# Kernel optimization log

Measured on AMD Instinct MI355X. Metric: run time of the kernel, lower is better.

The kernel has to match this reference:

```python
import jax, jax.numpy as jnp
import numpy as np

B, S, E = 4, 2048, 1024
H, D = 16, 64
SCALE = D ** -0.5


def setup_inputs() -> dict:
    key = jax.random.key(0)
    ks = jax.random.split(key, 9)
    std = E ** -0.5
    return {
        "hidden_states": jax.random.normal(ks[0], (B, S, E), jnp.float32),
        "Wq": jax.random.normal(ks[1], (E, E), jnp.float32) * std,
        "bq": jax.random.normal(ks[2], (E,), jnp.float32) * 0.02,
        "Wk": jax.random.normal(ks[3], (E, E), jnp.float32) * std,
        "bk": jax.random.normal(ks[4], (E,), jnp.float32) * 0.02,
        "Wv": jax.random.normal(ks[5], (E, E), jnp.float32) * std,
        "bv": jax.random.normal(ks[6], (E,), jnp.float32) * 0.02,
        "Wo": jax.random.normal(ks[7], (E, E), jnp.float32) * std,
        "bo": jax.random.normal(ks[8], (E,), jnp.float32) * 0.02,
    }


def reference(hidden_states, Wq, bq, Wk, bk, Wv, bv, Wo, bo):
    b, s, e = hidden_states.shape
    # projections (torch Linear: x @ W^T + b); query pre-scaled as in source
    q = (hidden_states @ Wq.T + bq) * SCALE
    k = hidden_states @ Wk.T + bk
    v = hidden_states @ Wv.T + bv
    # [b, s, h, d] -> [b, h, s, d]
    q = q.reshape(b, s, H, D).transpose(0, 2, 1, 3)
    k = k.reshape(b, s, H, D).transpose(0, 2, 1, 3)
    v = v.reshape(b, s, H, D).transpose(0, 2, 1, 3)
    # explicit QK^T, fp32 softmax (matches source: softmax in float32 then cast back)
    scores = jnp.einsum("bhqd,bhkd->bhqk", q, k)
    attn = jax.nn.softmax(scores.astype(jnp.float32), axis=-1).astype(q.dtype)
    out = jnp.einsum("bhqk,bhkd->bhqd", attn, v)
    out = out.transpose(0, 2, 1, 3).reshape(b, s, e)
    return out @ Wo.T + bo
```

## Files before the change

kernel.cpp:

```cpp
#include <hip/hip_runtime.h>
#include <hip/hip_bf16.h>

#define BB 4
#define SS 2048
#define EE 1024
#define HH 16
#define DD 64
static constexpr float SCALE = 0.125f;

typedef __attribute__((ext_vector_type(8))) short bf16x8;
typedef __attribute__((ext_vector_type(4))) float f32x4;

#define MFMA(a, b, c) __builtin_amdgcn_mfma_f32_16x16x32_bf16(a, b, c, 0, 0, 0)

#define GLDS16(gptr, lptr) __builtin_amdgcn_global_load_lds( \
    (const __attribute__((address_space(1))) unsigned int*)(gptr), \
    (__attribute__((address_space(3))) unsigned int*)(lptr), 16, 0, 0)

__device__ inline unsigned short f2bfu(float f) {
    __hip_bfloat16 h = __float2bfloat16(f);
    return *reinterpret_cast<unsigned short*>(&h);
}

#define NX4 2097152
#define NW4 262144
#define NT4 (NX4 + 4 * NW4)
__global__ __launch_bounds__(256) void cast_all(
    const float* __restrict__ X,  const float* __restrict__ Wq,
    const float* __restrict__ Wk, const float* __restrict__ Wv,
    const float* __restrict__ Wo, unsigned short* __restrict__ dst) {
    for (int i = blockIdx.x * 256 + threadIdx.x; i < NT4; i += gridDim.x * 256) {
        const float* src; int off;
        if (i < NX4)               { src = X;  off = i; }
        else if (i < NX4 + NW4)    { src = Wq; off = i - NX4; }
        else if (i < NX4 + 2*NW4)  { src = Wk; off = i - NX4 - NW4; }
        else if (i < NX4 + 3*NW4)  { src = Wv; off = i - NX4 - 2*NW4; }
        else                       { src = Wo; off = i - NX4 - 3*NW4; }
        float4 v = *(const float4*)(src + (size_t)off * 4);
        ushort4 o;
        o.x = f2bfu(v.x); o.y = f2bfu(v.y); o.z = f2bfu(v.z); o.w = f2bfu(v.w);
        *(ushort4*)(dst + (size_t)i * 4) = o;
    }
}

__global__ __launch_bounds__(256) void qkv_gemm(
    const unsigned short* __restrict__ A, const unsigned short* __restrict__ Bw,
    const float* __restrict__ bq, const float* __restrict__ bk,
    const float* __restrict__ bv,
    unsigned short* __restrict__ Qo, unsigned short* __restrict__ Ko,
    unsigned short* __restrict__ Vo)
{
    __shared__ __align__(16) unsigned short As[3][4096];
    __shared__ __align__(16) unsigned short Bs[3][4096];

    const int tid = threadIdx.x;
    const int lane = tid & 63, wave = tid >> 6;
    const int l15 = lane & 15, quad = lane >> 4;
    const int wr = (wave & 1) * 64, wc = (wave >> 1) * 64;
    const int m0 = blockIdx.y * 128, n0 = blockIdx.x * 128;

    const int c0 = tid,        r0 = c0 >> 2, g0 = (c0 & 3) ^ ((r0 >> 1) & 3);
    const int c1 = tid + 256,  r1 = c1 >> 2, g1 = (c1 & 3) ^ ((r1 >> 1) & 3);

    const unsigned short* aG0 = A  + (size_t)(m0 + r0) * 1024 + g0 * 8;
    const unsigned short* aG1 = A  + (size_t)(m0 + r1) * 1024 + g1 * 8;
    const unsigned short* bG0 = Bw + (size_t)(n0 + r0) * 1024 + g0 * 8;
    const unsigned short* bG1 = Bw + (size_t)(n0 + r1) * 1024 + g1 * 8;

    const int aBase = (wr + l15) * 4 + (quad ^ (((wr + l15) >> 1) & 3));
    const int bBase = (wc + l15) * 4 + (quad ^ (((wc + l15) >> 1) & 3));

    f32x4 acc[4][4] = {};

#define QSTAGE(t_, buf_) do {                                              \
        const int k_ = (t_) * 32;                                          \
        GLDS16(aG0 + k_, (char*)As[buf_] + tid * 16);                      \
        GLDS16(aG1 + k_, (char*)As[buf_] + 4096 + tid * 16);               \
        GLDS16(bG0 + k_, (char*)Bs[buf_] + tid * 16);                      \
        GLDS16(bG1 + k_, (char*)Bs[buf_] + 4096 + tid * 16);               \
    } while (0)

    QSTAGE(0, 0);
    QSTAGE(1, 1);
    asm volatile("s_waitcnt vmcnt(4)" ::: "memory");
    __syncthreads();

    int cur = 0, nxt = 2;
    for (int t = 0; t < 32; ++t) {
        if (t < 30) QSTAGE(t + 2, nxt);

        bf16x8 af[4], bf[4];
        #pragma unroll
        for (int u = 0; u < 4; ++u) {
            af[u] = *(const bf16x8*)(As[cur] + (aBase + u * 64) * 8);
            bf[u] = *(const bf16x8*)(Bs[cur] + (bBase + u * 64) * 8);
        }
        #pragma unroll
        for (int i = 0; i < 4; ++i)
            #pragma unroll
            for (int j = 0; j < 4; ++j)
                acc[i][j] = MFMA(af[i], bf[j], acc[i][j]);

        if (t < 30) asm volatile("s_waitcnt vmcnt(4)" ::: "memory");
        else        asm volatile("s_waitcnt vmcnt(0)" ::: "memory");
        __syncthreads();
        cur = cur == 2 ? 0 : cur + 1;
        nxt = nxt == 2 ? 0 : nxt + 1;
    }
#undef QSTAGE

    const int which = n0 >> 10;
    const float* __restrict__ bia = which == 0 ? bq : which == 1 ? bk : bv;
    unsigned short* __restrict__ dst = which == 0 ? Qo : which == 1 ? Ko : Vo;
    const float sc = which == 0 ? SCALE : 1.f;

    #pragma unroll
    for (int j = 0; j < 4; ++j) {
        const int nn = (n0 + wc + j * 16 + l15) & 1023;
        const float bval = bia[nn];
        const int h = nn >> 6, d = nn & 63;
        #pragma unroll
        for (int i = 0; i < 4; ++i) {
            #pragma unroll
            for (int r = 0; r < 4; ++r) {
                const int m = m0 + wr + i * 16 + quad * 4 + r;
                const int b = m >> 11, s = m & 2047;
                const size_t idx = (which == 2)
                    ? ((size_t)(b * 16 + h) * 64 + d) * 2048 + s
                    : ((size_t)(b * 16 + h) * 2048 + s) * 64 + d;
                dst[idx] = f2bfu((acc[i][j][r] + bval) * sc);
            }
        }
    }
}

__global__ __launch_bounds__(256) void out_gemm(
    const unsigned short* __restrict__ A, const unsigned short* __restrict__ Bw,
    const float* __restrict__ bo, float* __restrict__ out)
{
    __shared__ __align__(16) unsigned short As[3][4096];
    __shared__ __align__(16) unsigned short Bs[3][4096];

    const int tid = threadIdx.x;
    const int lane = tid & 63, wave = tid >> 6;
    const int l15 = lane & 15, quad = lane >> 4;
    const int wr = (wave & 1) * 64, wc = (wave >> 1) * 64;
    const int m0 = blockIdx.y * 128, n0 = blockIdx.x * 128;

    const int c0 = tid,        r0 = c0 >> 2, g0 = (c0 & 3) ^ ((r0 >> 1) & 3);
    const int c1 = tid + 256,  r1 = c1 >> 2, g1 = (c1 & 3) ^ ((r1 >> 1) & 3);

    const unsigned short* aG0 = A  + (size_t)(m0 + r0) * 1024 + g0 * 8;
    const unsigned short* aG1 = A  + (size_t)(m0 + r1) * 1024 + g1 * 8;
    const unsigned short* bG0 = Bw + (size_t)(n0 + r0) * 1024 + g0 * 8;
    const unsigned short* bG1 = Bw + (size_t)(n0 + r1) * 1024 + g1 * 8;

    const int aBase = (wr + l15) * 4 + (quad ^ (((wr + l15) >> 1) & 3));
    const int bBase = (wc + l15) * 4 + (quad ^ (((wc + l15) >> 1) & 3));

    f32x4 acc[4][4] = {};

#define OSTAGE(t_, buf_) do {                                              \
        const int k_ = (t_) * 32;                                          \
        GLDS16(aG0 + k_, (char*)As[buf_] + tid * 16);                      \
        GLDS16(aG1 + k_, (char*)As[buf_] + 4096 + tid * 16);               \
        GLDS16(bG0 + k_, (char*)Bs[buf_] + tid * 16);                      \
        GLDS16(bG1 + k_, (char*)Bs[buf_] + 4096 + tid * 16);               \
    } while (0)

    OSTAGE(0, 0);
    OSTAGE(1, 1);
    asm volatile("s_waitcnt vmcnt(4)" ::: "memory");
    __syncthreads();

    int cur = 0, nxt = 2;
    for (int t = 0; t < 32; ++t) {
        if (t < 30) OSTAGE(t + 2, nxt);

        bf16x8 af[4], bf[4];
        #pragma unroll
        for (int u = 0; u < 4; ++u) {
            af[u] = *(const bf16x8*)(As[cur] + (aBase + u * 64) * 8);
            bf[u] = *(const bf16x8*)(Bs[cur] + (bBase + u * 64) * 8);
        }
        #pragma unroll
        for (int i = 0; i < 4; ++i)
            #pragma unroll
            for (int j = 0; j < 4; ++j)
                acc[i][j] = MFMA(af[i], bf[j], acc[i][j]);

        if (t < 30) asm volatile("s_waitcnt vmcnt(4)" ::: "memory");
        else        asm volatile("s_waitcnt vmcnt(0)" ::: "memory");
        __syncthreads();
        cur = cur == 2 ? 0 : cur + 1;
        nxt = nxt == 2 ? 0 : nxt + 1;
    }
#undef OSTAGE

    #pragma unroll
    for (int j = 0; j < 4; ++j) {
        const int n = n0 + wc + j * 16 + l15;
        const float bval = bo[n];
        #pragma unroll
        for (int i = 0; i < 4; ++i) {
            #pragma unroll
            for (int r = 0; r < 4; ++r) {
                const int m = m0 + wr + i * 16 + quad * 4 + r;
                out[(size_t)m * 1024 + n] = acc[i][j][r] + bval;
            }
        }
    }
}

__global__ __launch_bounds__(512, 8) void flash_attn(
    const unsigned short* __restrict__ Qg, const unsigned short* __restrict__ Kg,
    const unsigned short* __restrict__ Vg, unsigned short* __restrict__ AO)
{
    __shared__ __align__(16) unsigned short Ks[4096];
    __shared__ __align__(16) unsigned short Vt[64 * 72];
    __shared__ __align__(16) unsigned short Ps[128 * 72];

    const int tid = threadIdx.x;
    const int lane = tid & 63, wave = tid >> 6;
    const int l15 = lane & 15, quad = lane >> 4;

    const int x = blockIdx.x & 7, j = blockIdx.x >> 3;
    const int bh = x * 8 + (j >> 4);
    const int q0 = (j & 15) * 128;

    const size_t baseK = (size_t)bh * SS * DD;
    const size_t baseV = (size_t)bh * DD * SS;

    bf16x8 qa[2];
    #pragma unroll
    for (int kc = 0; kc < 2; ++kc)
        qa[kc] = *(const bf16x8*)(Qg + baseK +
            (size_t)(q0 + wave * 16 + l15) * 64 + kc * 32 + quad * 8);

    f32x4 oacc[4] = {};
    float psum = 0.f;

    const int kkg = tid >> 6, kky = tid & 63;
    const int vr  = tid >> 3, vc  = tid & 7;

    uint4 tk = *(const uint4*)(Kg + baseK + (size_t)kky * 64 + kkg * 8);
    uint4 tv = *(const uint4*)(Vg + baseV + (size_t)vr * 2048 + vc * 8);

    for (int kt = 0; kt < 32; ++kt) {
        __syncthreads();
        *(uint4*)(Ks + tid * 8) = tk;
        *(uint4*)(Vt + vr * 72 + vc * 8) = tv;
        __syncthreads();

        if (kt < 31) {
            const int krow = (kt + 1) * 64;
            tk = *(const uint4*)(Kg + baseK + (size_t)(krow + kky) * 64 + kkg * 8);
            tv = *(const uint4*)(Vg + baseV + (size_t)vr * 2048 + krow + vc * 8);
        }

        const int prow = (wave * 16 + l15) * 72;
        #pragma unroll
        for (int ct = 0; ct < 4; ++ct) {
            f32x4 s = {};
            __builtin_amdgcn_s_setprio(1);
            #pragma unroll
            for (int kc = 0; kc < 2; ++kc) {
                bf16x8 kb = *(const bf16x8*)(Ks +
                    ((kc * 4 + quad) * 64 + ct * 16 + l15) * 8);
                s = MFMA(kb, qa[kc], s);
            }
            __builtin_amdgcn_s_setprio(0);
            const float e0 = __expf(s[0]), e1 = __expf(s[1]);
            const float e2 = __expf(s[2]), e3 = __expf(s[3]);
            psum += (e0 + e1) + (e2 + e3);
            ushort4 p;
            p.x = f2bfu(e0); p.y = f2bfu(e1); p.z = f2bfu(e2); p.w = f2bfu(e3);
            *(ushort4*)(Ps + prow + ct * 16 + quad * 4) = p;
        }

        __builtin_amdgcn_s_setprio(1);
        #pragma unroll
        for (int k4 = 0; k4 < 2; ++k4) {
            bf16x8 pa = *(const bf16x8*)(Ps +
                (wave * 16 + l15) * 72 + k4 * 32 + quad * 8);
            #pragma unroll
            for (int dt = 0; dt < 4; ++dt) {
                bf16x8 vb = *(const bf16x8*)(Vt +
                    (dt * 16 + l15) * 72 + k4 * 32 + quad * 8);
                oacc[dt] = MFMA(pa, vb, oacc[dt]);
            }
        }
        __builtin_amdgcn_s_setprio(0);
    }

    const int b = bh >> 4, h = bh & 15;
    float tot = psum;
    tot += __shfl_xor(tot, 16);
    tot += __shfl_xor(tot, 32);
    float inv[4];
    #pragma unroll
    for (int r = 0; r < 4; ++r)
        inv[r] = 1.f / __shfl(tot, quad * 4 + r);
    const int srow = q0 + wave * 16 + quad * 4;
    #pragma unroll
    for (int dt = 0; dt < 4; ++dt) {
        const int col = h * 64 + dt * 16 + l15;
        #pragma unroll
        for (int r = 0; r < 4; ++r)
            AO[((size_t)b * 2048 + srow + r) * 1024 + col] =
                f2bfu(oacc[dt][r] * inv[r]);
    }
}

extern "C" void kernel_launch(void* const* d_in, const int* in_sizes, int n_in,
                              void* d_out, int out_size, void* d_ws, size_t ws_size,
                              hipStream_t stream) {
    const float* X  = (const float*)d_in[0];
    const float* Wq = (const float*)d_in[1];
    const float* bq = (const float*)d_in[2];
    const float* Wk = (const float*)d_in[3];
    const float* bk = (const float*)d_in[4];
    const float* Wv = (const float*)d_in[5];
    const float* bv = (const float*)d_in[6];
    const float* Wo = (const float*)d_in[7];
    const float* bo = (const float*)d_in[8];
    float* out = (float*)d_out;

    unsigned short* w = (unsigned short*)d_ws;
    unsigned short* Xb  = w;
    unsigned short* Wb  = Xb  + 8388608;
    unsigned short* Wob = Wb  + 3145728;
    unsigned short* Qb  = Wob + 1048576;
    unsigned short* Kb  = Qb  + 8388608;
    unsigned short* Vb  = Kb  + 8388608;
    unsigned short* AOb = Vb  + 8388608;

    cast_all<<<2048, 256, 0, stream>>>(X, Wq, Wk, Wv, Wo, Xb);
    qkv_gemm<<<dim3(24, 64), 256, 0, stream>>>(Xb, Wb, bq, bk, bv, Qb, Kb, Vb);
    flash_attn<<<dim3(1024), 512, 0, stream>>>(Qb, Kb, Vb, AOb);
    out_gemm<<<dim3(8, 64), 256, 0, stream>>>(AOb, Wob, bo, out);
}
```

Measured before the change: 310.8 us.

## Use 32x32 MFMA in attention and keep P in registers via permlane swap

```diff
diff --git a/kernel.cpp b/kernel.cpp
--- a/kernel.cpp
+++ b/kernel.cpp
@@ -10,8 +10,10 @@
 
 typedef __attribute__((ext_vector_type(8))) short bf16x8;
 typedef __attribute__((ext_vector_type(4))) float f32x4;
-
-#define MFMA(a, b, c) __builtin_amdgcn_mfma_f32_16x16x32_bf16(a, b, c, 0, 0, 0)
+typedef __attribute__((ext_vector_type(16))) float f32x16;
+
+#define MFMA(a, b, c)   __builtin_amdgcn_mfma_f32_16x16x32_bf16(a, b, c, 0, 0, 0)
+#define MFMA32(a, b, c) __builtin_amdgcn_mfma_f32_32x32x16_bf16(a, b, c, 0, 0, 0)
 
 #define GLDS16(gptr, lptr) __builtin_amdgcn_global_load_lds( \
     (const __attribute__((address_space(1))) unsigned int*)(gptr), \
@@ -20,6 +22,12 @@
 __device__ inline unsigned short f2bfu(float f) {
     __hip_bfloat16 h = __float2bfloat16(f);
     return *reinterpret_cast<unsigned short*>(&h);
+}
+
+__device__ inline unsigned cvtpk(float lo, float hi) {
+    unsigned r;
+    asm("v_cvt_pk_bf16_f32 %0, %1, %2" : "=v"(r) : "v"(lo), "v"(hi));
+    return r;
 }
 
 #define NX4 2097152
@@ -212,17 +220,16 @@
     }
 }
 
-__global__ __launch_bounds__(512, 8) void flash_attn(
+__global__ __launch_bounds__(256, 4) void flash_attn(
     const unsigned short* __restrict__ Qg, const unsigned short* __restrict__ Kg,
     const unsigned short* __restrict__ Vg, unsigned short* __restrict__ AO)
 {
     __shared__ __align__(16) unsigned short Ks[4096];
     __shared__ __align__(16) unsigned short Vt[64 * 72];
-    __shared__ __align__(16) unsigned short Ps[128 * 72];
 
     const int tid = threadIdx.x;
     const int lane = tid & 63, wave = tid >> 6;
-    const int l15 = lane & 15, quad = lane >> 4;
+    const int l31 = lane & 31, half = lane >> 5;
 
     const int x = blockIdx.x & 7, j = blockIdx.x >> 3;
     const int bh = x * 8 + (j >> 4);
@@ -231,84 +238,106 @@
     const size_t baseK = (size_t)bh * SS * DD;
     const size_t baseV = (size_t)bh * DD * SS;
 
-    bf16x8 qa[2];
-    #pragma unroll
-    for (int kc = 0; kc < 2; ++kc)
-        qa[kc] = *(const bf16x8*)(Qg + baseK +
-            (size_t)(q0 + wave * 16 + l15) * 64 + kc * 32 + quad * 8);
-
-    f32x4 oacc[4] = {};
+    bf16x8 qa[4];
+    #pragma unroll
+    for (int m = 0; m < 4; ++m)
+        qa[m] = *(const bf16x8*)(Qg + baseK +
+            (size_t)(q0 + wave * 32 + l31) * 64 + m * 16 + half * 8);
+
+    f32x16 oacc[2] = {};
     float psum = 0.f;
 
-    const int kkg = tid >> 6, kky = tid & 63;
-    const int vr  = tid >> 3, vc  = tid & 7;
-
-    uint4 tk = *(const uint4*)(Kg + baseK + (size_t)kky * 64 + kkg * 8);
-    uint4 tv = *(const uint4*)(Vg + baseV + (size_t)vr * 2048 + vc * 8);
+    int kkg[2], kky[2], vr[2], vc[2];
+    #pragma unroll
+    for (int i = 0; i < 2; ++i) {
+        const int c = tid + i * 256;
+        kkg[i] = c >> 6; kky[i] = c & 63;
+        vr[i]  = c >> 3; vc[i]  = c & 7;
+    }
+
+    uint4 tk[2], tv[2];
+    #pragma unroll
+    for (int i = 0; i < 2; ++i) {
+        tk[i] = *(const uint4*)(Kg + baseK + (size_t)kky[i] * 64 + kkg[i] * 8);
+        tv[i] = *(const uint4*)(Vg + baseV + (size_t)vr[i] * 2048 + vc[i] * 8);
+    }
 
     for (int kt = 0; kt < 32; ++kt) {
         __syncthreads();
-        *(uint4*)(Ks + tid * 8) = tk;
-        *(uint4*)(Vt + vr * 72 + vc * 8) = tv;
+        #pragma unroll
+        for (int i = 0; i < 2; ++i) {
+            *(uint4*)(Ks + (tid + i * 256) * 8) = tk[i];
+            *(uint4*)(Vt + vr[i] * 72 + vc[i] * 8) = tv[i];
+        }
         __syncthreads();
 
         if (kt < 31) {
             const int krow = (kt + 1) * 64;
-            tk = *(const uint4*)(Kg + baseK + (size_t)(krow + kky) * 64 + kkg * 8);
-            tv = *(const uint4*)(Vg + baseV + (size_t)vr * 2048 + krow + vc * 8);
-        }
-
-        const int prow = (wave * 16 + l15) * 72;
-        #pragma unroll
-        for (int ct = 0; ct < 4; ++ct) {
-            f32x4 s = {};
+            #pragma unroll
+            for (int i = 0; i < 2; ++i) {
+                tk[i] = *(const uint4*)(Kg + baseK +
+                        (size_t)(krow + kky[i]) * 64 + kkg[i] * 8);
+                tv[i] = *(const uint4*)(Vg + baseV +
+                        (size_t)vr[i] * 2048 + krow + vc[i] * 8);
+            }
+        }
+
+        #pragma unroll
+        for (int t32 = 0; t32 < 2; ++t32) {
+            f32x16 s = {};
             __builtin_amdgcn_s_setprio(1);
             #pragma unroll
-            for (int kc = 0; kc < 2; ++kc) {
+            for (int m = 0; m < 4; ++m) {
                 bf16x8 kb = *(const bf16x8*)(Ks +
-                    ((kc * 4 + quad) * 64 + ct * 16 + l15) * 8);
-                s = MFMA(kb, qa[kc], s);
+                    ((2 * m + half) * 64 + t32 * 32 + l31) * 8);
+                s = MFMA32(kb, qa[m], s);
             }
             __builtin_amdgcn_s_setprio(0);
-            const float e0 = __expf(s[0]), e1 = __expf(s[1]);
-            const float e2 = __expf(s[2]), e3 = __expf(s[3]);
-            psum += (e0 + e1) + (e2 + e3);
-            ushort4 p;
-            p.x = f2bfu(e0); p.y = f2bfu(e1); p.z = f2bfu(e2); p.w = f2bfu(e3);
-            *(ushort4*)(Ps + prow + ct * 16 + quad * 4) = p;
-        }
-
-        __builtin_amdgcn_s_setprio(1);
-        #pragma unroll
-        for (int k4 = 0; k4 < 2; ++k4) {
-            bf16x8 pa = *(const bf16x8*)(Ps +
-                (wave * 16 + l15) * 72 + k4 * 32 + quad * 8);
-            #pragma unroll
-            for (int dt = 0; dt < 4; ++dt) {
-                bf16x8 vb = *(const bf16x8*)(Vt +
-                    (dt * 16 + l15) * 72 + k4 * 32 + quad * 8);
-                oacc[dt] = MFMA(pa, vb, oacc[dt]);
-            }
-        }
-        __builtin_amdgcn_s_setprio(0);
+
+            float e[16];
+            #pragma unroll
+            for (int r = 0; r < 16; ++r) {
+                e[r] = __expf(s[r]);
+                psum += e[r];
+            }
+
+            __builtin_amdgcn_s_setprio(1);
+            #pragma unroll
+            for (int g = 0; g < 2; ++g) {
+                unsigned c01 = cvtpk(e[g*8+0], e[g*8+1]);
+                unsigned c23 = cvtpk(e[g*8+2], e[g*8+3]);
+                unsigned c45 = cvtpk(e[g*8+4], e[g*8+5]);
+                unsigned c67 = cvtpk(e[g*8+6], e[g*8+7]);
+                unsigned a0 = c01, b0 = c45, a1 = c23, b1 = c67;
+                asm volatile("v_permlane32_swap_b32 %0, %1" : "+v"(a0), "+v"(b0));
+                asm volatile("v_permlane32_swap_b32 %0, %1" : "+v"(a1), "+v"(b1));
+                union { unsigned u[4]; bf16x8 v8; } pu;
+                pu.u[0] = a0; pu.u[1] = a1; pu.u[2] = b0; pu.u[3] = b1;
+                const int mk = t32 * 2 + g;
+                #pragma unroll
+                for (int dt = 0; dt < 2; ++dt) {
+                    bf16x8 vb = *(const bf16x8*)(Vt +
+                        (l31 + 32 * dt) * 72 + mk * 16 + half * 8);
+                    oacc[dt] = MFMA32(pu.v8, vb, oacc[dt]);
+                }
+            }
+            __builtin_amdgcn_s_setprio(0);
+        }
     }
 
     const int b = bh >> 4, h = bh & 15;
-    float tot = psum;
-    tot += __shfl_xor(tot, 16);
-    tot += __shfl_xor(tot, 32);
-    float inv[4];
-    #pragma unroll
-    for (int r = 0; r < 4; ++r)
-        inv[r] = 1.f / __shfl(tot, quad * 4 + r);
-    const int srow = q0 + wave * 16 + quad * 4;
-    #pragma unroll
-    for (int dt = 0; dt < 4; ++dt) {
-        const int col = h * 64 + dt * 16 + l15;
-        #pragma unroll
-        for (int r = 0; r < 4; ++r)
-            AO[((size_t)b * 2048 + srow + r) * 1024 + col] =
-                f2bfu(oacc[dt][r] * inv[r]);
+    const float tot = psum + __shfl_xor(psum, 32);
+    const float inv = 1.f / tot;
+    #pragma unroll
+    for (int r = 0; r < 16; ++r) {
+        const int qloc = (r & 3) + 8 * (r >> 2) + 4 * half;
+        const float iv = __shfl(inv, qloc);
+        const int srow = q0 + wave * 32 + qloc;
+        #pragma unroll
+        for (int dt = 0; dt < 2; ++dt) {
+            AO[((size_t)b * 2048 + srow) * 1024 + h * 64 + dt * 32 + l31] =
+                f2bfu(oacc[dt][r] * iv);
+        }
     }
 }
 
@@ -337,6 +366,6 @@
 
     cast_all<<<2048, 256, 0, stream>>>(X, Wq, Wk, Wv, Wo, Xb);
     qkv_gemm<<<dim3(24, 64), 256, 0, stream>>>(Xb, Wb, bq, bk, bv, Qb, Kb, Vb);
-    flash_attn<<<dim3(1024), 512, 0, stream>>>(Qb, Kb, Vb, AOb);
+    flash_attn<<<dim3(1024), 256, 0, stream>>>(Qb, Kb, Vb, AOb);
     out_gemm<<<dim3(8, 64), 256, 0, stream>>>(AOb, Wob, bo, out);
 }
```

New measurement: 371.0 us. 19.3% more time.
